# Kernel optimization log

Measured on AMD Instinct MI355X. Metric: run time of the kernel, lower is better.

## Reference

```python
import jax, jax.numpy as jnp
import numpy as np

HEADS = 4
HD = 64  # per-head dim: hidden_dim // heads
NEG = 0.2  # PyG GATConv default negative_slope


def _gat(x, W, a_s, a_d, b, src, dst, n):
    # x: [N, in_dim]; W: [in_dim, heads*hd]
    h = (x @ W).reshape(-1, HEADS, HD)           # [N, H, D]
    es = jnp.einsum('nhd,hd->nh', h, a_s)        # [N, H]
    ed = jnp.einsum('nhd,hd->nh', h, a_d)
    e = jax.nn.leaky_relu(es[src] + ed[dst], NEG)  # [E, H]
    m = jax.ops.segment_max(e, dst, num_segments=n)
    m = jnp.where(jnp.isfinite(m), m, 0.0)
    ex = jnp.exp(e - m[dst])
    den = jax.ops.segment_sum(ex, dst, num_segments=n)
    alpha = ex / (den[dst] + 1e-16)              # segment softmax over incoming edges
    out = jax.ops.segment_sum(alpha[:, :, None] * h[src], dst, num_segments=n)
    return out.reshape(-1, HEADS * HD) + b


def _ln(x, g, b):
    mu = jnp.mean(x, -1, keepdims=True)
    v = jnp.var(x, -1, keepdims=True)
    return (x - mu) * jax.lax.rsqrt(v + 1e-5) * g + b


def _forward(text_features, image_features, user_emb_table, item_emb_table, ut_W, ut_b, ui_W, ui_b, it_W, it_b, ii_W, ii_b, ua_Wv, ua_bv, ua_Wo, ua_bo, ia_Wv, ia_bv, ia_Wo, ia_bo, gat_W0, gat_W1, gat_W2, att_src, att_dst, gat_b, res_W, res_b, ln_gamma, ln_beta, user_ids, item_ids, edge_index):
    B = user_ids.shape[0]
    Tn = text_features.shape[0]
    In = image_features.shape[0]
    ue = user_emb_table[user_ids]                # [B, 256]
    ie = item_emb_table[item_ids]
    ut = text_features[user_ids % Tn] @ ut_W + ut_b
    ui = image_features[user_ids % In] @ ui_W + ui_b
    it = text_features[item_ids % Tn] @ it_W + it_b
    ii = image_features[item_ids % In] @ ii_W + ii_b
    um = jnp.concatenate([ut, ui], 1)            # [B, 256]
    im = jnp.concatenate([it, ii], 1)
    # MultiheadAttention with seq_len==1: softmax over one key is identity,
    # so output == out_proj(v_proj(x)).
    ua = (um @ ua_Wv + ua_bv) @ ua_Wo + ua_bo
    ia = (im @ ia_Wv + ia_bv) @ ia_Wo + ia_bo
    x = jnp.concatenate([jnp.concatenate([ue, ua], 1), jnp.concatenate([ie, ia], 1)], 0)  # [2B, 512]
    src, dst = edge_index[0], edge_index[1]
    n = 2 * B
    Ws = [gat_W0, gat_W1, gat_W2]
    for i in range(3):
        if i > 0:
            x = x + (x @ res_W[i - 1] + res_b[i - 1])
        x = _gat(x, Ws[i], att_src[i], att_dst[i], gat_b[i], src, dst, n)
        x = jax.nn.relu(_ln(x, ln_gamma[i], ln_beta[i]))
    u = x[:B]
    v = x[B:2 * B]
    return jnp.sum(u * v, 1), u, v


def setup_inputs():
    key = jax.random.key(0)
    ks = jax.random.split(key, 24)
    B = 65536; E = 524288; Tn = 32768; NU = 100000; NI = 50000
    def rn(k, shape, fan):
        return jax.random.normal(k, shape, jnp.float32) * np.float32(1.0 / np.sqrt(fan))
    d = {}
    d['text_features'] = jax.random.normal(ks[0], (Tn, 1000), jnp.float32)
    d['image_features'] = jax.random.normal(ks[1], (Tn, 512), jnp.float32)
    d['user_emb_table'] = rn(ks[2], (NU, 256), 256)
    d['item_emb_table'] = rn(ks[3], (NI, 256), 256)
    d['ut_W'] = rn(ks[4], (1000, 128), 1000); d['ut_b'] = jnp.zeros((128,), jnp.float32)
    d['ui_W'] = rn(ks[5], (512, 128), 512); d['ui_b'] = jnp.zeros((128,), jnp.float32)
    d['it_W'] = rn(ks[6], (1000, 128), 1000); d['it_b'] = jnp.zeros((128,), jnp.float32)
    d['ii_W'] = rn(ks[7], (512, 128), 512); d['ii_b'] = jnp.zeros((128,), jnp.float32)
    d['ua_Wv'] = rn(ks[8], (256, 256), 256); d['ua_bv'] = jnp.zeros((256,), jnp.float32)
    d['ua_Wo'] = rn(ks[9], (256, 256), 256); d['ua_bo'] = jnp.zeros((256,), jnp.float32)
    d['ia_Wv'] = rn(ks[10], (256, 256), 256); d['ia_bv'] = jnp.zeros((256,), jnp.float32)
    d['ia_Wo'] = rn(ks[11], (256, 256), 256); d['ia_bo'] = jnp.zeros((256,), jnp.float32)
    d['gat_W0'] = rn(ks[12], (512, 256), 512)
    d['gat_W1'] = rn(ks[13], (256, 256), 256)
    d['gat_W2'] = rn(ks[14], (256, 256), 256)
    d['att_src'] = rn(ks[15], (3, 4, 64), 64)
    d['att_dst'] = rn(ks[16], (3, 4, 64), 64)
    d['gat_b'] = jnp.zeros((3, 256), jnp.float32)
    d['res_W'] = rn(ks[17], (2, 256, 256), 256)
    d['res_b'] = jnp.zeros((2, 256), jnp.float32)
    d['ln_gamma'] = jnp.ones((3, 256), jnp.float32)
    d['ln_beta'] = jnp.zeros((3, 256), jnp.float32)
    d['user_ids'] = jax.random.randint(ks[18], (B,), 0, NU, jnp.int32)
    d['item_ids'] = jax.random.randint(ks[19], (B,), 0, NI, jnp.int32)
    d['edge_index'] = jax.random.randint(ks[20], (2, E), 0, 2 * B, jnp.int32)
    return d


def reference(text_features, image_features, user_emb_table, item_emb_table, ut_W, ut_b, ui_W, ui_b, it_W, it_b, ii_W, ii_b, ua_Wv, ua_bv, ua_Wo, ua_bo, ia_Wv, ia_bv, ia_Wo, ia_bo, gat_W0, gat_W1, gat_W2, att_src, att_dst, gat_b, res_W, res_b, ln_gamma, ln_beta, user_ids, item_ids, edge_index):
    return _forward(text_features, image_features, user_emb_table, item_emb_table, ut_W, ut_b, ui_W, ui_b, it_W, it_b, ii_W, ii_b, ua_Wv, ua_bv, ua_Wo, ua_bo, ia_Wv, ia_bv, ia_Wo, ia_bo, gat_W0, gat_W1, gat_W2, att_src, att_dst, gat_b, res_W, res_b, ln_gamma, ln_beta, user_ids, item_ids, edge_index)
```

## Files before the change

kernel.cpp:

```cpp
#include <hip/hip_runtime.h>
#include <hip/hip_bf16.h>
#include <cmath>
#include <cstdint>
#include <cstddef>

#define NEG 0.2f

typedef __attribute__((ext_vector_type(8))) short bf16x8;
typedef __attribute__((ext_vector_type(4))) float f32x4;

__device__ __forceinline__ unsigned pack2(float a, float b) {
  __hip_bfloat162 t = __float22bfloat162_rn(make_float2(a, b));
  return *reinterpret_cast<unsigned*>(&t);
}
__device__ __forceinline__ float2 unpack2(unsigned w) {
  __hip_bfloat162 t = *reinterpret_cast<__hip_bfloat162*>(&w);
  return __bfloat1622float2(t);
}

__global__ __launch_bounds__(256) void gemm_k(
    const float* __restrict__ A, int lda,
    const int* __restrict__ ids, int mod,
    const unsigned short* __restrict__ Wh, const unsigned short* __restrict__ Wl,
    int ldk, int wcolBase, const float* __restrict__ bias,
    float* __restrict__ C, int ldc, int ccolBase,
    int K, int mode, int flags,
    const float* __restrict__ uemb, const float* __restrict__ iemb,
    const int* __restrict__ uids, const int* __restrict__ iids,
    const float* __restrict__ att, int Busers)
{
  __shared__ unsigned short Ah[128 * 40];
  __shared__ unsigned short Al[128 * 40];
  __shared__ unsigned short Bh[128 * 40];
  __shared__ unsigned short Bl[128 * 40];

  const int tid = threadIdx.x;
  const int m0 = blockIdx.x * 128;
  const int wcol = wcolBase + blockIdx.y * 128;
  const int ccol = ccolBase + blockIdx.y * 128;

  const int rr = tid >> 1, q = tid & 1;

  const int wid = tid >> 6;
  const int l = tid & 63;
  const int wr = wid >> 1, wc = wid & 1;
  const int lr = l & 15;
  const int kb = l >> 4;

  int aoff[4], boff[4];
#pragma unroll
  for (int i = 0; i < 4; ++i) {
    aoff[i] = (wr * 64 + i * 16 + lr) * 40 + kb * 8;
    boff[i] = (wc * 64 + i * 16 + lr) * 40 + kb * 8;
  }

  f32x4 acc[4][4];
#pragma unroll
  for (int mi = 0; mi < 4; ++mi)
#pragma unroll
    for (int ni = 0; ni < 4; ++ni) acc[mi][ni] = (f32x4)0.f;

  const float* arow = nullptr;
  const float* arow2 = nullptr;
  {
    const int row = m0 + rr;
    if (mode == 1) {
      const int gid = (int)(((unsigned)ids[row]) % (unsigned)mod);
      arow = A + (size_t)gid * lda;
    } else if (mode == 0) {
      arow = A + (size_t)row * lda;
    } else {
      if (row < Busers) arow = uemb + (size_t)uids[row] * 256;
      else              arow = iemb + (size_t)iids[row - Busers] * 256;
      arow2 = att + (size_t)row * 256;
    }
  }

  for (int k0 = 0; k0 < K; k0 += 32) {
    {
      const float* sp; int kk;
      if (mode == 2) {
        if (k0 < 256) { sp = arow;  kk = k0; }
        else          { sp = arow2; kk = k0 - 256; }
      } else { sp = arow; kk = k0; }
      float f[16];
      if (k0 + 32 <= K) {
        const float4 x0 = *(const float4*)(sp + kk + q * 16);
        const float4 x1 = *(const float4*)(sp + kk + q * 16 + 4);
        const float4 x2 = *(const float4*)(sp + kk + q * 16 + 8);
        const float4 x3 = *(const float4*)(sp + kk + q * 16 + 12);
        f[0]=x0.x; f[1]=x0.y; f[2]=x0.z; f[3]=x0.w;
        f[4]=x1.x; f[5]=x1.y; f[6]=x1.z; f[7]=x1.w;
        f[8]=x2.x; f[9]=x2.y; f[10]=x2.z; f[11]=x2.w;
        f[12]=x3.x; f[13]=x3.y; f[14]=x3.z; f[15]=x3.w;
      } else {
#pragma unroll
        for (int j = 0; j < 16; ++j) {
          const int kg = k0 + q * 16 + j;
          f[j] = (kg < K) ? sp[kk + q * 16 + j] : 0.f;
        }
      }
      unsigned hw[8], lw[8];
#pragma unroll
      for (int p = 0; p < 8; ++p) {
        const unsigned h = pack2(f[2*p], f[2*p+1]);
        const float2 hf = unpack2(h);
        lw[p] = pack2(f[2*p] - hf.x, f[2*p+1] - hf.y);
        hw[p] = h;
      }
      uint4 v;
      const int sb = rr * 40 + q * 16;
      v.x=hw[0]; v.y=hw[1]; v.z=hw[2]; v.w=hw[3]; *(uint4*)&Ah[sb] = v;
      v.x=hw[4]; v.y=hw[5]; v.z=hw[6]; v.w=hw[7]; *(uint4*)&Ah[sb + 8] = v;
      v.x=lw[0]; v.y=lw[1]; v.z=lw[2]; v.w=lw[3]; *(uint4*)&Al[sb] = v;
      v.x=lw[4]; v.y=lw[5]; v.z=lw[6]; v.w=lw[7]; *(uint4*)&Al[sb + 8] = v;
    }
    {
      const size_t wb = (size_t)(wcol + rr) * ldk + k0 + q * 16;
      const int sb = rr * 40 + q * 16;
      *(uint4*)&Bh[sb]     = *(const uint4*)(Wh + wb);
      *(uint4*)&Bh[sb + 8] = *(const uint4*)(Wh + wb + 8);
      *(uint4*)&Bl[sb]     = *(const uint4*)(Wl + wb);
      *(uint4*)&Bl[sb + 8] = *(const uint4*)(Wl + wb + 8);
    }
    __syncthreads();
    bf16x8 fah[4], fal[4], fbh[4], fbl[4];
#pragma unroll
    for (int i = 0; i < 4; ++i) {
      fah[i] = *(const bf16x8*)&Ah[aoff[i]];
      fal[i] = *(const bf16x8*)&Al[aoff[i]];
      fbh[i] = *(const bf16x8*)&Bh[boff[i]];
      fbl[i] = *(const bf16x8*)&Bl[boff[i]];
    }
#pragma unroll
    for (int mi = 0; mi < 4; ++mi)
#pragma unroll
      for (int ni = 0; ni < 4; ++ni) {
        acc[mi][ni] = __builtin_amdgcn_mfma_f32_16x16x32_bf16(fah[mi], fbh[ni], acc[mi][ni], 0, 0, 0);
        acc[mi][ni] = __builtin_amdgcn_mfma_f32_16x16x32_bf16(fah[mi], fbl[ni], acc[mi][ni], 0, 0, 0);
        acc[mi][ni] = __builtin_amdgcn_mfma_f32_16x16x32_bf16(fal[mi], fbh[ni], acc[mi][ni], 0, 0, 0);
      }
    __syncthreads();
  }

#pragma unroll
  for (int ni = 0; ni < 4; ++ni) {
    const int col = ccol + wc * 64 + ni * 16 + lr;
    const float bv = bias ? bias[wcol + wc * 64 + ni * 16 + lr] : 0.f;
#pragma unroll
    for (int mi = 0; mi < 4; ++mi) {
#pragma unroll
      for (int j = 0; j < 4; ++j) {
        const int row = m0 + wr * 64 + mi * 16 + kb * 4 + j;
        float o = acc[mi][ni][j] + bv;
        if (flags & 1) o += A[(size_t)row * lda + col];
        C[(size_t)row * ldc + col] = o;
      }
    }
  }
}

__global__ void wsplit_k(const float* __restrict__ W, int Ncols, int K,
                         int ldkShift, unsigned short* __restrict__ Wh,
                         unsigned short* __restrict__ Wl)
{
  const int i = blockIdx.x * 256 + threadIdx.x;
  const int ldk = 1 << ldkShift;
  const int n = i >> ldkShift;
  const int k = i & (ldk - 1);
  if (n >= Ncols) return;
  const float v = (k < K) ? W[(size_t)k * Ncols + n] : 0.f;
  const unsigned u = __float_as_uint(v);
  const unsigned r = u + 0x7fffu + ((u >> 16) & 1);
  const unsigned short h = (unsigned short)(r >> 16);
  const float hf = __uint_as_float(((unsigned)h) << 16);
  const float res = v - hf;
  const unsigned u2 = __float_as_uint(res);
  const unsigned r2 = u2 + 0x7fffu + ((u2 >> 16) & 1);
  Wh[i] = h;
  Wl[i] = (unsigned short)(r2 >> 16);
}

__global__ __launch_bounds__(256) void esed_k(const float* __restrict__ h,
    const float* __restrict__ as, const float* __restrict__ ad,
    float* __restrict__ es, float* __restrict__ ed, int n)
{
  const int wv = blockIdx.x * 4 + (threadIdx.x >> 6);
  const int lane = threadIdx.x & 63;
  if (wv >= n) return;
  const float4 hv = *(const float4*)(h + (size_t)wv * 256 + lane * 4);
  const int head = lane >> 4;
  const int doff = (lane & 15) * 4;
  const float* asp = as + head * 64 + doff;
  const float* adp = ad + head * 64 + doff;
  float ps = hv.x*asp[0] + hv.y*asp[1] + hv.z*asp[2] + hv.w*asp[3];
  float pd = hv.x*adp[0] + hv.y*adp[1] + hv.z*adp[2] + hv.w*adp[3];
#pragma unroll
  for (int mask = 1; mask < 16; mask <<= 1) {
    ps += __shfl_xor(ps, mask);
    pd += __shfl_xor(pd, mask);
  }
  if ((lane & 15) == 0) {
    es[(size_t)wv * 4 + head] = ps;
    ed[(size_t)wv * 4 + head] = pd;
  }
}

__global__ __launch_bounds__(256) void agg_k(const float* __restrict__ h,
    const float* __restrict__ es, const float* __restrict__ ed,
    const int* __restrict__ rowptr, const int* __restrict__ srclist,
    const float* __restrict__ gb, const float* __restrict__ gamma,
    const float* __restrict__ beta, float* __restrict__ xout, int n)
{
  const int wv = blockIdx.x * 4 + (threadIdx.x >> 6);
  const int lane = threadIdx.x & 63;
  if (wv >= n) return;
  const int head = lane >> 4;
  const int start = rowptr[wv], end = rowptr[wv + 1];
  const float edv = ed[(size_t)wv * 4 + head];
  float m = -INFINITY, den = 0.f;
  float ax = 0.f, ay = 0.f, az = 0.f, aw = 0.f;
  for (int p = start; p < end; ++p) {
    const int s = srclist[p];
    float ev = es[(size_t)s * 4 + head] + edv;
    ev = ev > 0.f ? ev : NEG * ev;
    const float nm = fmaxf(m, ev);
    const float sc = expf(m - nm);
    const float w = expf(ev - nm);
    den = den * sc + w;
    const float4 hv = *(const float4*)(h + (size_t)s * 256 + lane * 4);
    ax = ax * sc + w * hv.x;
    ay = ay * sc + w * hv.y;
    az = az * sc + w * hv.z;
    aw = aw * sc + w * hv.w;
    m = nm;
  }
  const float inv = 1.f / (den + 1e-16f);
  const int c = lane * 4;
  const float o0 = ax * inv + gb[c + 0];
  const float o1 = ay * inv + gb[c + 1];
  const float o2 = az * inv + gb[c + 2];
  const float o3 = aw * inv + gb[c + 3];
  float s1 = o0 + o1 + o2 + o3;
  float s2 = o0*o0 + o1*o1 + o2*o2 + o3*o3;
#pragma unroll
  for (int mask = 1; mask < 64; mask <<= 1) {
    s1 += __shfl_xor(s1, mask);
    s2 += __shfl_xor(s2, mask);
  }
  const float mu = s1 * (1.f / 256.f);
  const float var = s2 * (1.f / 256.f) - mu * mu;
  const float rs = rsqrtf(var + 1e-5f);
  float4 o;
  o.x = fmaxf(0.f, (o0 - mu) * rs * gamma[c + 0] + beta[c + 0]);
  o.y = fmaxf(0.f, (o1 - mu) * rs * gamma[c + 1] + beta[c + 1]);
  o.z = fmaxf(0.f, (o2 - mu) * rs * gamma[c + 2] + beta[c + 2]);
  o.w = fmaxf(0.f, (o3 - mu) * rs * gamma[c + 3] + beta[c + 3]);
  *(float4*)(xout + (size_t)wv * 256 + c) = o;
}

__global__ void zero_k(int* __restrict__ p, int n) {
  const int i = blockIdx.x * 256 + threadIdx.x;
  if (i < n) p[i] = 0;
}
__global__ void count_k(const int* __restrict__ dst, int* __restrict__ counts, int E) {
  const int e = blockIdx.x * 256 + threadIdx.x;
  if (e < E) atomicAdd(&counts[dst[e]], 1);
}
__global__ __launch_bounds__(256) void scan1_k(const int* __restrict__ counts,
    int* __restrict__ rowptr, int* __restrict__ bsums, int n)
{
  __shared__ int sd[256];
  const int tid = threadIdx.x;
  const int base = blockIdx.x * 1024 + tid * 4;
  int a0 = base + 0 < n ? counts[base + 0] : 0;
  int a1 = base + 1 < n ? counts[base + 1] : 0;
  int a2 = base + 2 < n ? counts[base + 2] : 0;
  int a3 = base + 3 < n ? counts[base + 3] : 0;
  const int t = a0 + a1 + a2 + a3;
  sd[tid] = t;
  __syncthreads();
  for (int off = 1; off < 256; off <<= 1) {
    int v = 0;
    if (tid >= off) v = sd[tid - off];
    __syncthreads();
    sd[tid] += v;
    __syncthreads();
  }
  const int excl = sd[tid] - t;
  if (base + 0 < n) rowptr[base + 0] = excl;
  if (base + 1 < n) rowptr[base + 1] = excl + a0;
  if (base + 2 < n) rowptr[base + 2] = excl + a0 + a1;
  if (base + 3 < n) rowptr[base + 3] = excl + a0 + a1 + a2;
  if (tid == 255) bsums[blockIdx.x] = sd[255];
}
__global__ __launch_bounds__(256) void scan2_k(int* __restrict__ bsums, int nb) {
  __shared__ int sd[256];
  const int tid = threadIdx.x;
  const int v = tid < nb ? bsums[tid] : 0;
  sd[tid] = v;
  __syncthreads();
  for (int off = 1; off < 256; off <<= 1) {
    int u = 0;
    if (tid >= off) u = sd[tid - off];
    __syncthreads();
    sd[tid] += u;
    __syncthreads();
  }
  if (tid < nb) bsums[tid] = sd[tid] - v;
}
__global__ void scan3_k(int* __restrict__ rowptr, const int* __restrict__ bsums,
                        int n, int E) {
  const int i = blockIdx.x * 256 + threadIdx.x;
  if (i < n) rowptr[i] += bsums[i >> 10];
  if (i == 0) rowptr[n] = E;
}
__global__ void copy_k(const int* __restrict__ a, int* __restrict__ b, int n) {
  const int i = blockIdx.x * 256 + threadIdx.x;
  if (i < n) b[i] = a[i];
}
__global__ void scatter_k(const int* __restrict__ srcA, const int* __restrict__ dstA,
                          int* __restrict__ cursor, int* __restrict__ srclist, int E) {
  const int e = blockIdx.x * 256 + threadIdx.x;
  if (e < E) {
    const int d = dstA[e];
    const int p = atomicAdd(&cursor[d], 1);
    srclist[p] = srcA[e];
  }
}

__global__ __launch_bounds__(256) void out_k(const float* __restrict__ x,
                                             float* __restrict__ out, int B)
{
  const int wv = blockIdx.x * 4 + (threadIdx.x >> 6);
  const int lane = threadIdx.x & 63;
  if (wv >= B) return;
  const float4 u = *(const float4*)(x + (size_t)wv * 256 + lane * 4);
  const float4 v = *(const float4*)(x + (size_t)(B + wv) * 256 + lane * 4);
  *(float4*)(out + (size_t)B + (size_t)wv * 256 + lane * 4) = u;
  *(float4*)(out + (size_t)B + (size_t)B * 256 + (size_t)wv * 256 + lane * 4) = v;
  float d = u.x*v.x + u.y*v.y + u.z*v.z + u.w*v.w;
#pragma unroll
  for (int mask = 1; mask < 64; mask <<= 1) d += __shfl_xor(d, mask);
  if (lane == 0) out[wv] = d;
}

extern "C" void kernel_launch(void* const* d_in, const int* in_sizes, int n_in,
                              void* d_out, int out_size, void* d_ws, size_t ws_size,
                              hipStream_t stream) {
  const float* text  = (const float*)d_in[0];
  const float* image = (const float*)d_in[1];
  const float* uemb  = (const float*)d_in[2];
  const float* iemb  = (const float*)d_in[3];
  const float* ut_W = (const float*)d_in[4];  const float* ut_b = (const float*)d_in[5];
  const float* ui_W = (const float*)d_in[6];  const float* ui_b = (const float*)d_in[7];
  const float* it_W = (const float*)d_in[8];  const float* it_b = (const float*)d_in[9];
  const float* ii_W = (const float*)d_in[10]; const float* ii_b = (const float*)d_in[11];
  const float* ua_Wv = (const float*)d_in[12]; const float* ua_bv = (const float*)d_in[13];
  const float* ua_Wo = (const float*)d_in[14]; const float* ua_bo = (const float*)d_in[15];
  const float* ia_Wv = (const float*)d_in[16]; const float* ia_bv = (const float*)d_in[17];
  const float* ia_Wo = (const float*)d_in[18]; const float* ia_bo = (const float*)d_in[19];
  const float* gat_W[3] = {(const float*)d_in[20], (const float*)d_in[21], (const float*)d_in[22]};
  const float* att_src = (const float*)d_in[23];
  const float* att_dst = (const float*)d_in[24];
  const float* gat_b   = (const float*)d_in[25];
  const float* res_W   = (const float*)d_in[26];
  const float* res_b   = (const float*)d_in[27];
  const float* ln_g    = (const float*)d_in[28];
  const float* ln_b    = (const float*)d_in[29];
  const int* user_ids = (const int*)d_in[30];
  const int* item_ids = (const int*)d_in[31];
  const int* edge     = (const int*)d_in[32];

  const int Tn = in_sizes[0] / 1000;
  const int In = in_sizes[1] / 512;
  const int B  = in_sizes[30];
  const int E  = in_sizes[32] / 2;
  const int n  = 2 * B;
  const int* esrc = edge;
  const int* edst = edge + E;

  const size_t F = (size_t)n * 256;
  float* tbuf = (float*)d_ws;
  float* hbuf = tbuf + F;
  float* xbuf = hbuf + F;
  float* es   = xbuf + F;
  float* ed   = es + (size_t)n * 4;
  int* counts  = (int*)(ed + (size_t)n * 4);
  int* rowptr  = counts + n;
  int* cursor  = rowptr + (n + 4);
  int* srclist = cursor + n;
  int* bsums   = srclist + E;
  unsigned short* WH = (unsigned short*)(bsums + 256);
  unsigned short* WL = WH + 1048576;
  const int nb = (n + 1023) / 1024;

  const dim3 blk(256);
  const float* NF = nullptr;
  const int* NI = nullptr;

  wsplit_k<<<dim3(512), blk, 0, stream>>>(ut_W, 128, 1000, 10, WH + 0,      WL + 0);
  wsplit_k<<<dim3(256), blk, 0, stream>>>(ui_W, 128, 512,  9,  WH + 131072, WL + 131072);
  wsplit_k<<<dim3(512), blk, 0, stream>>>(it_W, 128, 1000, 10, WH + 196608, WL + 196608);
  wsplit_k<<<dim3(256), blk, 0, stream>>>(ii_W, 128, 512,  9,  WH + 327680, WL + 327680);
  wsplit_k<<<dim3(256), blk, 0, stream>>>(ua_Wv, 256, 256, 8,  WH + 393216, WL + 393216);
  wsplit_k<<<dim3(256), blk, 0, stream>>>(ua_Wo, 256, 256, 8,  WH + 458752, WL + 458752);
  wsplit_k<<<dim3(256), blk, 0, stream>>>(ia_Wv, 256, 256, 8,  WH + 524288, WL + 524288);
  wsplit_k<<<dim3(256), blk, 0, stream>>>(ia_Wo, 256, 256, 8,  WH + 589824, WL + 589824);
  wsplit_k<<<dim3(512), blk, 0, stream>>>(gat_W[0], 256, 512, 9, WH + 655360, WL + 655360);
  wsplit_k<<<dim3(256), blk, 0, stream>>>(gat_W[1], 256, 256, 8, WH + 786432, WL + 786432);
  wsplit_k<<<dim3(256), blk, 0, stream>>>(gat_W[2], 256, 256, 8, WH + 851968, WL + 851968);
  wsplit_k<<<dim3(256), blk, 0, stream>>>(res_W,          256, 256, 8, WH + 917504, WL + 917504);
  wsplit_k<<<dim3(256), blk, 0, stream>>>(res_W + 65536,  256, 256, 8, WH + 983040, WL + 983040);

  gemm_k<<<dim3(B/128, 1), blk, 0, stream>>>(text, 1000, user_ids, Tn,
      WH + 0, WL + 0, 1024, 0, ut_b, tbuf, 256, 0, 1000, 1, 0, NF, NF, NI, NI, NF, 0);
  gemm_k<<<dim3(B/128, 1), blk, 0, stream>>>(image, 512, user_ids, In,
      WH + 131072, WL + 131072, 512, 0, ui_b, tbuf, 256, 128, 512, 1, 0, NF, NF, NI, NI, NF, 0);
  gemm_k<<<dim3(B/128, 1), blk, 0, stream>>>(text, 1000, item_ids, Tn,
      WH + 196608, WL + 196608, 1024, 0, it_b, tbuf + (size_t)B*256, 256, 0, 1000, 1, 0, NF, NF, NI, NI, NF, 0);
  gemm_k<<<dim3(B/128, 1), blk, 0, stream>>>(image, 512, item_ids, In,
      WH + 327680, WL + 327680, 512, 0, ii_b, tbuf + (size_t)B*256, 256, 128, 512, 1, 0, NF, NF, NI, NI, NF, 0);

  gemm_k<<<dim3(B/128, 2), blk, 0, stream>>>(tbuf, 256, NI, 0,
      WH + 393216, WL + 393216, 256, 0, ua_bv, hbuf, 256, 0, 256, 0, 0, NF, NF, NI, NI, NF, 0);
  gemm_k<<<dim3(B/128, 2), blk, 0, stream>>>(tbuf + (size_t)B*256, 256, NI, 0,
      WH + 524288, WL + 524288, 256, 0, ia_bv, hbuf + (size_t)B*256, 256, 0, 256, 0, 0, NF, NF, NI, NI, NF, 0);
  gemm_k<<<dim3(B/128, 2), blk, 0, stream>>>(hbuf, 256, NI, 0,
      WH + 458752, WL + 458752, 256, 0, ua_bo, tbuf, 256, 0, 256, 0, 0, NF, NF, NI, NI, NF, 0);
  gemm_k<<<dim3(B/128, 2), blk, 0, stream>>>(hbuf + (size_t)B*256, 256, NI, 0,
      WH + 589824, WL + 589824, 256, 0, ia_bo, tbuf + (size_t)B*256, 256, 0, 256, 0, 0, NF, NF, NI, NI, NF, 0);

  zero_k<<<dim3((n+255)/256), blk, 0, stream>>>(counts, n);
  count_k<<<dim3((E+255)/256), blk, 0, stream>>>(edst, counts, E);
  scan1_k<<<dim3(nb), blk, 0, stream>>>(counts, rowptr, bsums, n);
  scan2_k<<<dim3(1), blk, 0, stream>>>(bsums, nb);
  scan3_k<<<dim3((n+255)/256), blk, 0, stream>>>(rowptr, bsums, n, E);
  copy_k<<<dim3((n+255)/256), blk, 0, stream>>>(rowptr, cursor, n);
  scatter_k<<<dim3((E+255)/256), blk, 0, stream>>>(esrc, edst, cursor, srclist, E);

  for (int l = 0; l < 3; ++l) {
    if (l == 0) {
      gemm_k<<<dim3(n/128, 2), blk, 0, stream>>>(NF, 0, NI, 0,
          WH + 655360, WL + 655360, 512, 0, NF, hbuf, 256, 0, 512, 2, 0,
          uemb, iemb, user_ids, item_ids, tbuf, B);
    } else {
      const int roff = (l == 1) ? 917504 : 983040;
      gemm_k<<<dim3(n/128, 2), blk, 0, stream>>>(xbuf, 256, NI, 0,
          WH + roff, WL + roff, 256, 0, res_b + (size_t)(l-1)*256,
          tbuf, 256, 0, 256, 0, 1, NF, NF, NI, NI, NF, 0);
      const int goff = (l == 1) ? 786432 : 851968;
      gemm_k<<<dim3(n/128, 2), blk, 0, stream>>>(tbuf, 256, NI, 0,
          WH + goff, WL + goff, 256, 0, NF, hbuf, 256, 0, 256, 0, 0, NF, NF, NI, NI, NF, 0);
    }
    esed_k<<<dim3((n+3)/4), blk, 0, stream>>>(hbuf, att_src + (size_t)l*256,
        att_dst + (size_t)l*256, es, ed, n);
    agg_k<<<dim3((n+3)/4), blk, 0, stream>>>(hbuf, es, ed, rowptr, srclist,
        gat_b + (size_t)l*256, ln_g + (size_t)l*256, ln_b + (size_t)l*256, xbuf, n);
  }

  out_k<<<dim3((B+3)/4), blk, 0, stream>>>(xbuf, (float*)d_out, B);
}
```

Before: 1.977 ms.

## Prefetch next K-step into registers and use k-major LDS layout in GEMM

The GEMM main loop now issues global loads for the next K-slice into registers right after the barrier, so they overlap with the MFMA work on the current slice. The shared-memory tiles change from padded row-major [128][40] to a k-block-major [4][128][8] layout, which gives contiguous 16-byte fragment reads. The barrier placement moves so only one wait is needed before each store phase. This raises register pressure and may change LDS bank behaviour.

Result: no change. 2.000 ms (+1.2%).

```diff
diff --git a/kernel.cpp b/kernel.cpp
--- a/kernel.cpp
+++ b/kernel.cpp
@@ -29,10 +29,10 @@
     const int* __restrict__ uids, const int* __restrict__ iids,
     const float* __restrict__ att, int Busers)
 {
-  __shared__ unsigned short Ah[128 * 40];
-  __shared__ unsigned short Al[128 * 40];
-  __shared__ unsigned short Bh[128 * 40];
-  __shared__ unsigned short Bl[128 * 40];
+  __shared__ unsigned short Ah[4][128][8];
+  __shared__ unsigned short Al[4][128][8];
+  __shared__ unsigned short Bh[4][128][8];
+  __shared__ unsigned short Bl[4][128][8];
 
   const int tid = threadIdx.x;
   const int m0 = blockIdx.x * 128;
@@ -40,19 +40,13 @@
   const int ccol = ccolBase + blockIdx.y * 128;
 
   const int rr = tid >> 1, q = tid & 1;
+  const int kb0 = 2 * q, kb1 = 2 * q + 1;
 
   const int wid = tid >> 6;
   const int l = tid & 63;
   const int wr = wid >> 1, wc = wid & 1;
   const int lr = l & 15;
   const int kb = l >> 4;
-
-  int aoff[4], boff[4];
-#pragma unroll
-  for (int i = 0; i < 4; ++i) {
-    aoff[i] = (wr * 64 + i * 16 + lr) * 40 + kb * 8;
-    boff[i] = (wc * 64 + i * 16 + lr) * 40 + kb * 8;
-  }
 
   f32x4 acc[4][4];
 #pragma unroll
@@ -75,62 +69,72 @@
       arow2 = att + (size_t)row * 256;
     }
   }
-
-  for (int k0 = 0; k0 < K; k0 += 32) {
-    {
-      const float* sp; int kk;
-      if (mode == 2) {
-        if (k0 < 256) { sp = arow;  kk = k0; }
-        else          { sp = arow2; kk = k0 - 256; }
-      } else { sp = arow; kk = k0; }
-      float f[16];
-      if (k0 + 32 <= K) {
-        const float4 x0 = *(const float4*)(sp + kk + q * 16);
-        const float4 x1 = *(const float4*)(sp + kk + q * 16 + 4);
-        const float4 x2 = *(const float4*)(sp + kk + q * 16 + 8);
-        const float4 x3 = *(const float4*)(sp + kk + q * 16 + 12);
-        f[0]=x0.x; f[1]=x0.y; f[2]=x0.z; f[3]=x0.w;
-        f[4]=x1.x; f[5]=x1.y; f[6]=x1.z; f[7]=x1.w;
-        f[8]=x2.x; f[9]=x2.y; f[10]=x2.z; f[11]=x2.w;
-        f[12]=x3.x; f[13]=x3.y; f[14]=x3.z; f[15]=x3.w;
-      } else {
-#pragma unroll
-        for (int j = 0; j < 16; ++j) {
-          const int kg = k0 + q * 16 + j;
-          f[j] = (kg < K) ? sp[kk + q * 16 + j] : 0.f;
-        }
+  const size_t wbBase = (size_t)(wcol + rr) * ldk + q * 16;
+
+  float f[16];
+  uint4 rbh0, rbh1, rbl0, rbl1;
+
+  auto loadStep = [&](int s) {
+    const int k0 = s * 32;
+    const float* sp; int kk;
+    if (mode == 2) {
+      if (k0 < 256) { sp = arow;  kk = k0; }
+      else          { sp = arow2; kk = k0 - 256; }
+    } else { sp = arow; kk = k0; }
+    if (k0 + 32 <= K) {
+      const float4 x0 = *(const float4*)(sp + kk + q * 16);
+      const float4 x1 = *(const float4*)(sp + kk + q * 16 + 4);
+      const float4 x2 = *(const float4*)(sp + kk + q * 16 + 8);
+      const float4 x3 = *(const float4*)(sp + kk + q * 16 + 12);
+      f[0]=x0.x; f[1]=x0.y; f[2]=x0.z; f[3]=x0.w;
+      f[4]=x1.x; f[5]=x1.y; f[6]=x1.z; f[7]=x1.w;
+      f[8]=x2.x; f[9]=x2.y; f[10]=x2.z; f[11]=x2.w;
+      f[12]=x3.x; f[13]=x3.y; f[14]=x3.z; f[15]=x3.w;
+    } else {
+#pragma unroll
+      for (int j = 0; j < 16; ++j) {
+        const int kg = k0 + q * 16 + j;
+        f[j] = (kg < K) ? sp[kk + q * 16 + j] : 0.f;
       }
-      unsigned hw[8], lw[8];
-#pragma unroll
-      for (int p = 0; p < 8; ++p) {
-        const unsigned h = pack2(f[2*p], f[2*p+1]);
-        const float2 hf = unpack2(h);
-        lw[p] = pack2(f[2*p] - hf.x, f[2*p+1] - hf.y);
-        hw[p] = h;
-      }
-      uint4 v;
-      const int sb = rr * 40 + q * 16;
-      v.x=hw[0]; v.y=hw[1]; v.z=hw[2]; v.w=hw[3]; *(uint4*)&Ah[sb] = v;
-      v.x=hw[4]; v.y=hw[5]; v.z=hw[6]; v.w=hw[7]; *(uint4*)&Ah[sb + 8] = v;
-      v.x=lw[0]; v.y=lw[1]; v.z=lw[2]; v.w=lw[3]; *(uint4*)&Al[sb] = v;
-      v.x=lw[4]; v.y=lw[5]; v.z=lw[6]; v.w=lw[7]; *(uint4*)&Al[sb + 8] = v;
-    }
-    {
-      const size_t wb = (size_t)(wcol + rr) * ldk + k0 + q * 16;
-      const int sb = rr * 40 + q * 16;
-      *(uint4*)&Bh[sb]     = *(const uint4*)(Wh + wb);
-      *(uint4*)&Bh[sb + 8] = *(const uint4*)(Wh + wb + 8);
-      *(uint4*)&Bl[sb]     = *(const uint4*)(Wl + wb);
-      *(uint4*)&Bl[sb + 8] = *(const uint4*)(Wl + wb + 8);
-    }
+    }
+    const size_t wb = wbBase + k0;
+    rbh0 = *(const uint4*)(Wh + wb);
+    rbh1 = *(const uint4*)(Wh + wb + 8);
+    rbl0 = *(const uint4*)(Wl + wb);
+    rbl1 = *(const uint4*)(Wl + wb + 8);
+  };
+
+  const int nsteps = (K + 31) >> 5;
+  loadStep(0);
+
+  for (int s = 0; s < nsteps; ++s) {
+    unsigned hw[8], lw[8];
+#pragma unroll
+    for (int p = 0; p < 8; ++p) {
+      const unsigned h = pack2(f[2*p], f[2*p+1]);
+      const float2 hf = unpack2(h);
+      lw[p] = pack2(f[2*p] - hf.x, f[2*p+1] - hf.y);
+      hw[p] = h;
+    }
+    if (s) __syncthreads();
+    *(uint4*)&Ah[kb0][rr][0] = make_uint4(hw[0], hw[1], hw[2], hw[3]);
+    *(uint4*)&Ah[kb1][rr][0] = make_uint4(hw[4], hw[5], hw[6], hw[7]);
+    *(uint4*)&Al[kb0][rr][0] = make_uint4(lw[0], lw[1], lw[2], lw[3]);
+    *(uint4*)&Al[kb1][rr][0] = make_uint4(lw[4], lw[5], lw[6], lw[7]);
+    *(uint4*)&Bh[kb0][rr][0] = rbh0;
+    *(uint4*)&Bh[kb1][rr][0] = rbh1;
+    *(uint4*)&Bl[kb0][rr][0] = rbl0;
+    *(uint4*)&Bl[kb1][rr][0] = rbl1;
     __syncthreads();
+    if (s + 1 < nsteps) loadStep(s + 1);
+
     bf16x8 fah[4], fal[4], fbh[4], fbl[4];
 #pragma unroll
     for (int i = 0; i < 4; ++i) {
-      fah[i] = *(const bf16x8*)&Ah[aoff[i]];
-      fal[i] = *(const bf16x8*)&Al[aoff[i]];
-      fbh[i] = *(const bf16x8*)&Bh[boff[i]];
-      fbl[i] = *(const bf16x8*)&Bl[boff[i]];
+      fah[i] = *(const bf16x8*)&Ah[kb][wr * 64 + i * 16 + lr][0];
+      fal[i] = *(const bf16x8*)&Al[kb][wr * 64 + i * 16 + lr][0];
+      fbh[i] = *(const bf16x8*)&Bh[kb][wc * 64 + i * 16 + lr][0];
+      fbl[i] = *(const bf16x8*)&Bl[kb][wc * 64 + i * 16 + lr][0];
     }
 #pragma unroll
     for (int mi = 0; mi < 4; ++mi)
@@ -140,7 +144,6 @@
         acc[mi][ni] = __builtin_amdgcn_mfma_f32_16x16x32_bf16(fah[mi], fbl[ni], acc[mi][ni], 0, 0, 0);
         acc[mi][ni] = __builtin_amdgcn_mfma_f32_16x16x32_bf16(fal[mi], fbh[ni], acc[mi][ni], 0, 0, 0);
       }
-    __syncthreads();
   }
 
 #pragma unroll
```
